# Performance work log

Hardware: AMD Instinct MI355X
Metric: run time of the kernel (lower is better)

The kernel has to match this reference:

```python
import jax, jax.numpy as jnp
import numpy as np

N, E = 100000, 3200000
IN, HID, OUT, ED = 16, 64, 32, 3
BN_EPS = 1e-5


def setup_inputs() -> dict:
    key = jax.random.key(0)
    ks = jax.random.split(key, 40)
    d = {}
    d["x"] = jax.random.normal(ks[0], (N, IN), jnp.float32)
    d["edge_index"] = jax.random.randint(ks[1], (2, E), 0, N, dtype=jnp.int32)
    d["edge_attr"] = jax.random.normal(ks[2], (E, ED), jnp.float32)
    i = [3]
    def p(shape):
        w = jax.random.normal(ks[i[0]], shape, jnp.float32) * 0.05
        i[0] += 1
        return w
    for tag, nd in (("inj1", IN), ("inj2", HID), ("inj3", HID)):
        d[tag + "_w1"] = p((ED, nd)); d[tag + "_b1"] = p((nd,))
        d[tag + "_w2"] = p((nd, nd)); d[tag + "_b2"] = p((nd,))
    for tag, ci, co in (("conv1", IN, HID), ("conv2", HID, HID), ("conv3", HID, OUT)):
        d[tag + "_wl"] = p((ci, co)); d[tag + "_bl"] = p((co,))
        d[tag + "_wr"] = p((ci, co))
    for tag, c in (("bn1", HID), ("bn2", HID), ("bn3", OUT)):
        d[tag + "_w"] = p((c,)); d[tag + "_b"] = p((c,))
    return d


def _inject(x, src, dst, edge_attr, w1, b1, w2, b2):
    # edge MLP: [E, ED] -> [E, node_dim], sigmoid wind gate from column 2
    h = jax.nn.relu(edge_attr @ w1 + b1) @ w2 + b2
    gate = jax.nn.sigmoid(edge_attr[:, 2:3])
    msg = h * gate
    agg = jax.ops.segment_sum(msg, dst, num_segments=x.shape[0])
    return x + agg


def _sage(x, src, dst, wl, bl, wr):
    # PyG SAGEConv (mean aggr): lin_l(mean_{j in N(i)} x_j) + lin_r(x_i)
    n = x.shape[0]
    s = jax.ops.segment_sum(x[src], dst, num_segments=n)
    cnt = jax.ops.segment_sum(jnp.ones((src.shape[0], 1), x.dtype), dst, num_segments=n)
    mean = s / jnp.maximum(cnt, 1.0)
    return mean @ wl + bl + x @ wr


def _bn(x, w, b):
    # eval-mode BatchNorm with running_mean=0, running_var=1
    return x * (w / jnp.sqrt(1.0 + BN_EPS)) + b


def reference(x, edge_index, edge_attr,
              inj1_w1, inj1_b1, inj1_w2, inj1_b2,
              inj2_w1, inj2_b1, inj2_w2, inj2_b2,
              inj3_w1, inj3_b1, inj3_w2, inj3_b2,
              conv1_wl, conv1_bl, conv1_wr,
              conv2_wl, conv2_bl, conv2_wr,
              conv3_wl, conv3_bl, conv3_wr,
              bn1_w, bn1_b, bn2_w, bn2_b, bn3_w, bn3_b):
    src, dst = edge_index[0], edge_index[1]
    h = _inject(x, src, dst, edge_attr, inj1_w1, inj1_b1, inj1_w2, inj1_b2)
    h = jax.nn.relu(_bn(_sage(h, src, dst, conv1_wl, conv1_bl, conv1_wr), bn1_w, bn1_b))
    h = _inject(h, src, dst, edge_attr, inj2_w1, inj2_b1, inj2_w2, inj2_b2)
    h = jax.nn.relu(_bn(_sage(h, src, dst, conv2_wl, conv2_bl, conv2_wr), bn2_w, bn2_b))
    h = _inject(h, src, dst, edge_attr, inj3_w1, inj3_b1, inj3_w2, inj3_b2)
    h = jax.nn.relu(_bn(_sage(h, src, dst, conv3_wl, conv3_bl, conv3_wr), bn3_w, bn3_b))
    return h
```

## Files before the change

kernel.cpp:

```cpp
#include <hip/hip_runtime.h>
#include <math.h>

#define N_NODES 100000
#define N_EDGES 3200000
#define NB 391
#define CHUNK 4096
#define NCHUNK 782
#define HCHUNK 4096
#define NHCHUNK 782
#define CAPB 10240

constexpr size_t al512(size_t x){ return (x + 511) & ~size_t(511); }
constexpr size_t o_bcnt = 0;
constexpr size_t o_bst  = al512(o_bcnt + 512*4);
constexpr size_t o_gb   = al512(o_bst  + 512*4);
constexpr size_t o_off  = al512(o_gb   + 512*4);
constexpr size_t o_srcp = al512(o_off  + ((size_t)N_NODES+1)*4);
constexpr size_t o_epk  = al512(o_srcp + (size_t)N_EDGES*4);
constexpr size_t o_U1   = al512(o_epk  + (size_t)N_EDGES*16);
constexpr size_t o_U2   = al512(o_U1   + (size_t)N_NODES*16*4);
constexpr size_t o_U3   = o_U2 + (size_t)N_NODES*64*4;
constexpr size_t o_gs   = al512(o_U3   + (size_t)N_NODES*64*4);
constexpr size_t o_h1   = al512(o_gs   + (size_t)N_NODES*4);
constexpr size_t o_m1   = al512(o_h1   + (size_t)N_NODES*16*4);
constexpr size_t o_rec  = o_U2;
constexpr size_t o_h2bf = o_epk;
constexpr size_t o_h3bf = o_epk + (size_t)N_NODES*128;
constexpr size_t o_m2   = o_U2;
constexpr size_t o_y3   = o_U3;
constexpr size_t o_m3p  = o_U2;

#define BN_RSQRT 0.9999950000374997f

__device__ __forceinline__ float4 ld4(const float* p){ return *(const float4*)p; }
__device__ __forceinline__ float fc(const float4& v, int i){ return ((const float*)&v)[i]; }
__device__ __forceinline__ float uf(unsigned u){ return __uint_as_float(u); }

__device__ __forceinline__ unsigned f2bf(float x){
    unsigned u = __float_as_uint(x);
    u += 0x7fffu + ((u >> 16) & 1u);
    return u >> 16;
}

__global__ __launch_bounds__(256) void khistBin(const int* __restrict__ dst,
                                                int* __restrict__ binCnt){
    __shared__ int c[NB];
    int t = threadIdx.x;
    for(int i=t; i<NB; i+=256) c[i] = 0;
    __syncthreads();
    long base = (long)blockIdx.x*HCHUNK;
    int nrem = (int)(N_EDGES - base); if(nrem > HCHUNK) nrem = HCHUNK;
    for(int k=t; k<nrem; k+=256)
        atomicAdd(&c[dst[base+k] >> 8], 1);
    __syncthreads();
    for(int i=t; i<NB; i+=256)
        if(c[i]) atomicAdd(&binCnt[i], c[i]);
}

__global__ __launch_bounds__(512) void kscanBin(const int* __restrict__ binCnt,
                                                int* __restrict__ binStart,
                                                int* __restrict__ gbase){
    __shared__ int s[512];
    int t = threadIdx.x;
    int v = (t < NB) ? binCnt[t] : 0;
    s[t] = v; __syncthreads();
    for(int off=1; off<512; off<<=1){
        int a = (t>=off) ? s[t-off] : 0;
        __syncthreads(); s[t] += a; __syncthreads();
    }
    int ex = (t==0) ? 0 : s[t-1];
    if(t < NB){ binStart[t] = ex; gbase[t] = ex; }
    if(t == NB) binStart[NB] = s[NB-1];
}

__global__ __launch_bounds__(256) void kbinA(const int* __restrict__ src,
                                             const int* __restrict__ dst,
                                             const float* __restrict__ ea,
                                             int* __restrict__ gbase,
                                             unsigned* __restrict__ recD){
    __shared__ int cnt[NB], lofs[NB], gst[NB], lcnt[NB];
    __shared__ int sscan[256];
    __shared__ unsigned stage[CHUNK*3];
    __shared__ unsigned short binOf[CHUNK];
    int t = threadIdx.x;
    long e0i = (long)blockIdx.x*CHUNK;
    int nrem = (int)(N_EDGES - e0i); if(nrem > CHUNK) nrem = CHUNK;
    if(nrem <= 0) return;

    for(int b=t; b<NB; b+=256){ cnt[b]=0; lcnt[b]=0; }
    __syncthreads();
    for(int k=t; k<nrem; k+=256)
        atomicAdd(&cnt[dst[e0i+k] >> 8], 1);
    __syncthreads();
    int c0 = (2*t   < NB) ? cnt[2*t]   : 0;
    int c1 = (2*t+1 < NB) ? cnt[2*t+1] : 0;
    sscan[t] = c0 + c1;
    __syncthreads();
    for(int off=1; off<256; off<<=1){
        int v = (t>=off) ? sscan[t-off] : 0;
        __syncthreads(); sscan[t] += v; __syncthreads();
    }
    int base = (t==0) ? 0 : sscan[t-1];
    if(2*t   < NB) lofs[2*t]   = base;
    if(2*t+1 < NB) lofs[2*t+1] = base + c0;
    for(int b=t; b<NB; b+=256){
        int c = cnt[b];
        gst[b] = c ? atomicAdd(&gbase[b], c) : 0;
    }
    __syncthreads();
    for(int k=t; k<nrem; k+=256){
        long i = e0i + k;
        int d = dst[i];
        int s = src[i];
        float a0 = ea[i*3+0], a1 = ea[i*3+1], a2 = ea[i*3+2];
        int b = d >> 8;
        int p = lofs[b] + atomicAdd(&lcnt[b], 1);
        stage[3*p+0] = (unsigned)s | ((unsigned)(d & 255) << 17);
        stage[3*p+1] = (f2bf(a1)<<16) | f2bf(a0);
        stage[3*p+2] = __float_as_uint(a2);
        binOf[p] = (unsigned short)b;
    }
    __syncthreads();
    int total3 = nrem*3;
    for(int q=t; q<total3; q+=256){
        int p = q/3;
        int r = q - 3*p;
        int b = binOf[p];
        int g = gst[b] + (p - lofs[b]);
        recD[(size_t)3*g + r] = stage[q];
    }
}

__global__ __launch_bounds__(512) void kbinB(const unsigned* __restrict__ recD,
                                             const int* __restrict__ binStart,
                                             int* __restrict__ offs,
                                             int* __restrict__ srcp,
                                             float4* __restrict__ epk){
    __shared__ int pfx[257], lcnt[256];
    __shared__ int sscan[256];
    __shared__ unsigned short perm[CAPB];
    __shared__ unsigned char  nibOf[CAPB];
    int t = threadIdx.x;
    int b = blockIdx.x;
    int n0 = b*256;
    int nn = N_NODES - n0; if(nn > 256) nn = 256;
    int base = binStart[b];
    int m    = binStart[b+1] - base;
    for(int i=t; i<256; i+=512) lcnt[i] = 0;
    __syncthreads();
    for(int p=t; p<m; p+=512){
        unsigned w0 = recD[(size_t)3*(base+p)];
        int nib = (int)((w0 >> 17) & 255u);
        if(p < CAPB) nibOf[p] = (unsigned char)nib;
        atomicAdd(&lcnt[nib], 1);
    }
    __syncthreads();
    if(t < 256) sscan[t] = lcnt[t];
    __syncthreads();
    if(t < 256){
        for(int off=1; off<256; off<<=1){
            int v = (t>=off) ? sscan[t-off] : 0;
            __syncthreads(); sscan[t] += v; __syncthreads();
        }
        pfx[t+1] = sscan[t];
        if(t==0) pfx[0] = 0;
    } else {
        for(int off=1; off<256; off<<=1){ __syncthreads(); __syncthreads(); }
    }
    __syncthreads();
    for(int i=t; i<=nn; i+=512) offs[n0+i] = base + pfx[i];
    for(int i=t; i<256; i+=512) lcnt[i] = 0;
    __syncthreads();
    for(int p=t; p<m; p+=512){
        int nib = nibOf[p];
        int slot = pfx[nib] + atomicAdd(&lcnt[nib], 1);
        perm[slot] = (unsigned short)p;
    }
    __syncthreads();
    for(int s=t; s<m; s+=512){
        size_t q = (size_t)3*(base + (int)perm[s]);
        unsigned w0 = recD[q], w1 = recD[q+1], w2 = recD[q+2];
        float e2 = uf(w2);
        float gate = __builtin_amdgcn_rcpf(1.f + __expf(-e2));
        srcp[base+s] = (int)(w0 & 0x1FFFFu);
        epk [base+s] = make_float4(uf(w1<<16), uf(w1 & 0xffff0000u), e2, gate);
    }
}

__global__ __launch_bounds__(256) void kinject(const float4* __restrict__ epk, const int* __restrict__ offs,
                        const float* __restrict__ w11, const float* __restrict__ b11,
                        const float* __restrict__ w12, const float* __restrict__ b12,
                        const float* __restrict__ w13, const float* __restrict__ b13,
                        float* __restrict__ U1, float* __restrict__ U2,
                        float* __restrict__ U3, float* __restrict__ gsum){
    int gid = blockIdx.x*blockDim.x + threadIdx.x;
    int node = gid >> 6;
    if(node >= N_NODES) return;
    int lane = threadIdx.x & 63;
    int q = lane >> 4, j = lane & 15;
    float wa1=w11[j], wb1=w11[16+j], wc1=w11[32+j], bb1=b11[j];
    float wa2[4], wb2[4], wc2[4], bv2[4], wa3[4], wb3[4], wc3[4], bv3[4];
    #pragma unroll
    for(int k=0;k<4;k++){
        int c = j + 16*k;
        wa2[k]=w12[c]; wb2[k]=w12[64+c]; wc2[k]=w12[128+c]; bv2[k]=b12[c];
        wa3[k]=w13[c]; wb3[k]=w13[64+c]; wc3[k]=w13[128+c]; bv3[k]=b13[c];
    }
    int beg = offs[node], end = offs[node+1];
    float a1=0.f, g=0.f;
    float a2[4] = {0.f,0.f,0.f,0.f};
    float a3[4] = {0.f,0.f,0.f,0.f};
    for(int e=beg; e<end; e+=8){
        int ee0 = e + q, ee1 = e + 4 + q;
        float4 r0 = make_float4(0.f,0.f,0.f,0.f);
        float4 r1 = make_float4(0.f,0.f,0.f,0.f);
        if(ee0 < end) r0 = epk[ee0];
        if(ee1 < end) r1 = epk[ee1];
        {
            float h = fmaf(r0.z,wc1, fmaf(r0.y,wb1, fmaf(r0.x,wa1, bb1)));
            a1 = fmaf(fmaxf(h,0.f), r0.w, a1);
            #pragma unroll
            for(int k=0;k<4;k++){
                float h2 = fmaf(r0.z,wc2[k], fmaf(r0.y,wb2[k], fmaf(r0.x,wa2[k], bv2[k])));
                a2[k] = fmaf(fmaxf(h2,0.f), r0.w, a2[k]);
                float h3 = fmaf(r0.z,wc3[k], fmaf(r0.y,wb3[k], fmaf(r0.x,wa3[k], bv3[k])));
                a3[k] = fmaf(fmaxf(h3,0.f), r0.w, a3[k]);
            }
            g += r0.w;
        }
        {
            float h = fmaf(r1.z,wc1, fmaf(r1.y,wb1, fmaf(r1.x,wa1, bb1)));
            a1 = fmaf(fmaxf(h,0.f), r1.w, a1);
            #pragma unroll
            for(int k=0;k<4;k++){
                float h2 = fmaf(r1.z,wc2[k], fmaf(r1.y,wb2[k], fmaf(r1.x,wa2[k], bv2[k])));
                a2[k] = fmaf(fmaxf(h2,0.f), r1.w, a2[k]);
                float h3 = fmaf(r1.z,wc3[k], fmaf(r1.y,wb3[k], fmaf(r1.x,wa3[k], bv3[k])));
                a3[k] = fmaf(fmaxf(h3,0.f), r1.w, a3[k]);
            }
            g += r1.w;
        }
    }
    #pragma unroll
    for(int k=0;k<4;k++){
        a2[k] += __shfl_xor(a2[k], 16); a2[k] += __shfl_xor(a2[k], 32);
        a3[k] += __shfl_xor(a3[k], 16); a3[k] += __shfl_xor(a3[k], 32);
    }
    a1 += __shfl_xor(a1, 16); a1 += __shfl_xor(a1, 32);
    g  += __shfl_xor(g, 16);  g  += __shfl_xor(g, 32);
    float v2 = (q==0) ? a2[0] : (q==1) ? a2[1] : (q==2) ? a2[2] : a2[3];
    float v3 = (q==0) ? a3[0] : (q==1) ? a3[1] : (q==2) ? a3[2] : a3[3];
    U2[(size_t)node*64 + lane] = v2;
    U3[(size_t)node*64 + lane] = v3;
    if(lane < 16) U1[node*16 + j] = a1;
    if(lane == 0) gsum[node] = g;
}

__global__ void kgather16(const float* __restrict__ h, const int* __restrict__ srcp,
                          const int* __restrict__ offs, float* __restrict__ m){
    int gid = blockIdx.x*blockDim.x + threadIdx.x;
    int node = gid >> 6;
    if(node >= N_NODES) return;
    int lane = threadIdx.x & 63;
    int q = lane >> 4, d = lane & 15;
    int beg = offs[node], end = offs[node+1];
    float acc = 0.f;
    for(int e=beg+q; e<end; e+=4) acc += h[(size_t)srcp[e]*16 + d];
    acc += __shfl_down(acc, 32);
    acc += __shfl_down(acc, 16);
    if(lane < 16){
        float c = fmaxf((float)(end-beg), 1.f);
        m[node*16 + lane] = acc / c;
    }
}

__global__ void kgather64bf(const unsigned* __restrict__ hbf, const int* __restrict__ srcp,
                            const int* __restrict__ offs, float* __restrict__ m){
    int gid = blockIdx.x*blockDim.x + threadIdx.x;
    int node = gid >> 6;
    if(node >= N_NODES) return;
    int lane = threadIdx.x & 63;
    int q = lane >> 4, j = lane & 15;
    int beg = offs[node], end = offs[node+1];
    float4 acc = make_float4(0.f,0.f,0.f,0.f);
    for(int e=beg; e<end; e+=4){
        int ee = e + q;
        if(ee < end){
            int s = srcp[ee];
            uint2 w = *(const uint2*)(hbf + (size_t)s*32 + 2*j);
            acc.x += uf(w.x<<16); acc.y += uf(w.x & 0xffff0000u);
            acc.z += uf(w.y<<16); acc.w += uf(w.y & 0xffff0000u);
        }
    }
    acc.x += __shfl_xor(acc.x,16); acc.x += __shfl_xor(acc.x,32);
    acc.y += __shfl_xor(acc.y,16); acc.y += __shfl_xor(acc.y,32);
    acc.z += __shfl_xor(acc.z,16); acc.z += __shfl_xor(acc.z,32);
    acc.w += __shfl_xor(acc.w,16); acc.w += __shfl_xor(acc.w,32);
    if(lane < 16){
        float inv = 1.f / fmaxf((float)(end-beg), 1.f);
        float4 o; o.x=acc.x*inv; o.y=acc.y*inv; o.z=acc.z*inv; o.w=acc.w*inv;
        *(float4*)(m + (size_t)node*64 + 4*j) = o;
    }
}

__global__ void kgather32bf(const unsigned* __restrict__ y3, const int* __restrict__ srcp,
                            const int* __restrict__ offs, float* __restrict__ m){
    int gid = blockIdx.x*blockDim.x + threadIdx.x;
    int node = gid >> 6;
    if(node >= N_NODES) return;
    int lane = threadIdx.x & 63;
    int q = lane >> 4, j = lane & 15;
    int beg = offs[node], end = offs[node+1];
    float ax=0.f, ay=0.f;
    for(int e=beg; e<end; e+=8){
        int ee0 = e + q, ee1 = e + 4 + q;
        if(ee0 < end){
            unsigned w = y3[(size_t)srcp[ee0]*16 + j];
            ax += uf(w<<16); ay += uf(w & 0xffff0000u);
        }
        if(ee1 < end){
            unsigned w = y3[(size_t)srcp[ee1]*16 + j];
            ax += uf(w<<16); ay += uf(w & 0xffff0000u);
        }
    }
    ax += __shfl_xor(ax,16); ax += __shfl_xor(ax,32);
    ay += __shfl_xor(ay,16); ay += __shfl_xor(ay,32);
    if(lane < 16){
        float inv = 1.f / fmaxf((float)(end-beg), 1.f);
        float2 o; o.x = ax*inv; o.y = ay*inv;
        *(float2*)(m + (size_t)node*32 + 2*j) = o;
    }
}


__global__ __launch_bounds__(256) void kdense0(const float* __restrict__ x, const float* __restrict__ U1,
                        const float* __restrict__ gs, const float* __restrict__ w2,
                        const float* __restrict__ b2, float* __restrict__ h1){
    __shared__ float sw[256];
    int t = threadIdx.x;
    sw[t] = w2[t];
    __syncthreads();
    int idx = blockIdx.x*256 + t;
    int n = idx >> 4, j = idx & 15;
    float acc = x[idx] + gs[n]*b2[j];
    const float4* row = (const float4*)(U1 + n*16);
    #pragma unroll
    for(int i4=0;i4<4;i4++){
        float4 r = row[i4];
        acc += r.x*sw[(i4*4+0)*16 + j];
        acc += r.y*sw[(i4*4+1)*16 + j];
        acc += r.z*sw[(i4*4+2)*16 + j];
        acc += r.w*sw[(i4*4+3)*16 + j];
    }
    h1[idx] = acc;
}

__global__ __launch_bounds__(256) void kdense1(const float* __restrict__ m1, const float* __restrict__ h1,
                        const float* __restrict__ U2, const float* __restrict__ gs,
                        const float* __restrict__ wl, const float* __restrict__ bl,
                        const float* __restrict__ wr,
                        const float* __restrict__ w2, const float* __restrict__ b2,
                        const float* __restrict__ bnw, const float* __restrict__ bnb,
                        unsigned* __restrict__ h2bf){
    __shared__ float4 swl[16*16];
    __shared__ float4 swr[16*16];
    __shared__ float4 sw2[64*16];
    int t = threadIdx.x;
    swl[t] = ((const float4*)wl)[t];
    swr[t] = ((const float4*)wr)[t];
    #pragma unroll
    for(int k=0;k<4;k++) sw2[t + 256*k] = ((const float4*)w2)[t + 256*k];
    __syncthreads();

    int w = t>>6, l = t&63;
    int jg = l&15, j0 = jg*4, ng = l>>4;
    int nb = blockIdx.x*64 + w*16 + ng*4;
    int nn[4];
    #pragma unroll
    for(int k=0;k<4;k++) nn[k] = (nb+k < N_NODES) ? nb+k : N_NODES-1;

    float a[4][4], b[4][4];
    float4 blv = ld4(bl + j0);
    float4 b2v = ld4(b2 + j0);
    #pragma unroll
    for(int k=0;k<4;k++){
        float g = gs[nn[k]];
        a[k][0]=blv.x; a[k][1]=blv.y; a[k][2]=blv.z; a[k][3]=blv.w;
        b[k][0]=g*b2v.x; b[k][1]=g*b2v.y; b[k][2]=g*b2v.z; b[k][3]=g*b2v.w;
    }
    #pragma unroll
    for(int i=0;i<16;i+=4){
        float4 rm[4], rh[4];
        #pragma unroll
        for(int k=0;k<4;k++){ rm[k] = ld4(m1 + nn[k]*16 + i); rh[k] = ld4(h1 + nn[k]*16 + i); }
        #pragma unroll
        for(int ii=0;ii<4;ii++){
            float4 wL = swl[(i+ii)*16 + jg];
            float4 wR = swr[(i+ii)*16 + jg];
            #pragma unroll
            for(int k=0;k<4;k++){
                float vm = fc(rm[k],ii), vh = fc(rh[k],ii);
                a[k][0] = fmaf(vm,wL.x, fmaf(vh,wR.x, a[k][0]));
                a[k][1] = fmaf(vm,wL.y, fmaf(vh,wR.y, a[k][1]));
                a[k][2] = fmaf(vm,wL.z, fmaf(vh,wR.z, a[k][2]));
                a[k][3] = fmaf(vm,wL.w, fmaf(vh,wR.w, a[k][3]));
            }
        }
    }
    #pragma unroll 4
    for(int i=0;i<64;i+=4){
        float4 ru[4];
        #pragma unroll
        for(int k=0;k<4;k++) ru[k] = ld4(U2 + (size_t)nn[k]*64 + i);
        #pragma unroll
        for(int ii=0;ii<4;ii++){
            float4 wv = sw2[(i+ii)*16 + jg];
            #pragma unroll
            for(int k=0;k<4;k++){
                float vu = fc(ru[k],ii);
                b[k][0] = fmaf(vu,wv.x,b[k][0]);
                b[k][1] = fmaf(vu,wv.y,b[k][1]);
                b[k][2] = fmaf(vu,wv.z,b[k][2]);
                b[k][3] = fmaf(vu,wv.w,b[k][3]);
            }
        }
    }
    float4 bw = ld4(bnw + j0), bb = ld4(bnb + j0);
    #pragma unroll
    for(int k=0;k<4;k++){
        if(nb+k < N_NODES){
            float ox = fmaxf(a[k][0]*(bw.x*BN_RSQRT)+bb.x,0.f) + b[k][0];
            float oy = fmaxf(a[k][1]*(bw.y*BN_RSQRT)+bb.y,0.f) + b[k][1];
            float oz = fmaxf(a[k][2]*(bw.z*BN_RSQRT)+bb.z,0.f) + b[k][2];
            float ow = fmaxf(a[k][3]*(bw.w*BN_RSQRT)+bb.w,0.f) + b[k][3];
            uint2 pk; pk.x = f2bf(ox) | (f2bf(oy)<<16); pk.y = f2bf(oz) | (f2bf(ow)<<16);
            *(uint2*)(h2bf + (size_t)(nb+k)*32 + (j0>>1)) = pk;
        }
    }
}

__global__ __launch_bounds__(256) void kdense2(const float* __restrict__ m2, const unsigned* __restrict__ h2bf,
                        const float* __restrict__ U3, const float* __restrict__ gs,
                        const float* __restrict__ wl, const float* __restrict__ bl,
                        const float* __restrict__ wr,
                        const float* __restrict__ w2, const float* __restrict__ b2,
                        const float* __restrict__ bnw, const float* __restrict__ bnb,
                        unsigned* __restrict__ h3bf){
    __shared__ float4 swl[64*16];
    __shared__ float4 swr[64*16];
    __shared__ float4 sw2[64*16];
    int t = threadIdx.x;
    #pragma unroll
    for(int k=0;k<4;k++){
        swl[t + 256*k] = ((const float4*)wl)[t + 256*k];
        swr[t + 256*k] = ((const float4*)wr)[t + 256*k];
        sw2[t + 256*k] = ((const float4*)w2)[t + 256*k];
    }
    __syncthreads();

    int w = t>>6, l = t&63;
    int jg = l&15, j0 = jg*4, ng = l>>4;
    int nb = blockIdx.x*64 + w*16 + ng*4;
    int nn[4];
    #pragma unroll
    for(int k=0;k<4;k++) nn[k] = (nb+k < N_NODES) ? nb+k : N_NODES-1;

    float a[4][4], b[4][4];
    float4 blv = ld4(bl + j0);
    float4 b2v = ld4(b2 + j0);
    #pragma unroll
    for(int k=0;k<4;k++){
        float g = gs[nn[k]];
        a[k][0]=blv.x; a[k][1]=blv.y; a[k][2]=blv.z; a[k][3]=blv.w;
        b[k][0]=g*b2v.x; b[k][1]=g*b2v.y; b[k][2]=g*b2v.z; b[k][3]=g*b2v.w;
    }
    #pragma unroll 4
    for(int i=0;i<64;i+=4){
        float4 rm[4], rh[4];
        #pragma unroll
        for(int k=0;k<4;k++){
            rm[k] = ld4(m2 + (size_t)nn[k]*64 + i);
            uint2 hw = *(const uint2*)(h2bf + (size_t)nn[k]*32 + (i>>1));
            rh[k].x = uf(hw.x<<16); rh[k].y = uf(hw.x & 0xffff0000u);
            rh[k].z = uf(hw.y<<16); rh[k].w = uf(hw.y & 0xffff0000u);
        }
        #pragma unroll
        for(int ii=0;ii<4;ii++){
            float4 wL = swl[(i+ii)*16 + jg];
            float4 wR = swr[(i+ii)*16 + jg];
            #pragma unroll
            for(int k=0;k<4;k++){
                float vm = fc(rm[k],ii), vh = fc(rh[k],ii);
                a[k][0] = fmaf(vm,wL.x, fmaf(vh,wR.x, a[k][0]));
                a[k][1] = fmaf(vm,wL.y, fmaf(vh,wR.y, a[k][1]));
                a[k][2] = fmaf(vm,wL.z, fmaf(vh,wR.z, a[k][2]));
                a[k][3] = fmaf(vm,wL.w, fmaf(vh,wR.w, a[k][3]));
            }
        }
    }
    #pragma unroll 4
    for(int i=0;i<64;i+=4){
        float4 ru[4];
        #pragma unroll
        for(int k=0;k<4;k++) ru[k] = ld4(U3 + (size_t)nn[k]*64 + i);
        #pragma unroll
        for(int ii=0;ii<4;ii++){
            float4 wv = sw2[(i+ii)*16 + jg];
            #pragma unroll
            for(int k=0;k<4;k++){
                float vu = fc(ru[k],ii);
                b[k][0] = fmaf(vu,wv.x,b[k][0]);
                b[k][1] = fmaf(vu,wv.y,b[k][1]);
                b[k][2] = fmaf(vu,wv.z,b[k][2]);
                b[k][3] = fmaf(vu,wv.w,b[k][3]);
            }
        }
    }
    float4 bw = ld4(bnw + j0), bb = ld4(bnb + j0);
    #pragma unroll
    for(int k=0;k<4;k++){
        if(nb+k < N_NODES){
            float ox = fmaxf(a[k][0]*(bw.x*BN_RSQRT)+bb.x,0.f) + b[k][0];
            float oy = fmaxf(a[k][1]*(bw.y*BN_RSQRT)+bb.y,0.f) + b[k][1];
            float oz = fmaxf(a[k][2]*(bw.z*BN_RSQRT)+bb.z,0.f) + b[k][2];
            float ow = fmaxf(a[k][3]*(bw.w*BN_RSQRT)+bb.w,0.f) + b[k][3];
            uint2 pk; pk.x = f2bf(ox) | (f2bf(oy)<<16); pk.y = f2bf(oz) | (f2bf(ow)<<16);
            *(uint2*)(h3bf + (size_t)(nb+k)*32 + (j0>>1)) = pk;
        }
    }
}

__global__ __launch_bounds__(256) void kproj3(const unsigned* __restrict__ h3bf,
                                              const float* __restrict__ wl,
                                              unsigned* __restrict__ y3){
    __shared__ float4 swl[64*8];
    int t = threadIdx.x;
    #pragma unroll
    for(int k=0;k<2;k++) swl[t + 256*k] = ((const float4*)wl)[t + 256*k];
    __syncthreads();

    int w = t>>6, l = t&63;
    int jg = l&7, j0 = jg*4, ng = l>>3;
    int nb = blockIdx.x*128 + w*32 + ng*4;
    int nn[4];
    #pragma unroll
    for(int k=0;k<4;k++) nn[k] = (nb+k < N_NODES) ? nb+k : N_NODES-1;

    float a[4][4];
    #pragma unroll
    for(int k=0;k<4;k++){ a[k][0]=0.f; a[k][1]=0.f; a[k][2]=0.f; a[k][3]=0.f; }
    #pragma unroll 4
    for(int i=0;i<64;i+=4){
        float4 rh[4];
        #pragma unroll
        for(int k=0;k<4;k++){
            uint2 hw = *(const uint2*)(h3bf + (size_t)nn[k]*32 + (i>>1));
            rh[k].x = uf(hw.x<<16); rh[k].y = uf(hw.x & 0xffff0000u);
            rh[k].z = uf(hw.y<<16); rh[k].w = uf(hw.y & 0xffff0000u);
        }
        #pragma unroll
        for(int ii=0;ii<4;ii++){
            float4 wL = swl[(i+ii)*8 + jg];
            #pragma unroll
            for(int k=0;k<4;k++){
                float vh = fc(rh[k],ii);
                a[k][0] = fmaf(vh,wL.x,a[k][0]);
                a[k][1] = fmaf(vh,wL.y,a[k][1]);
                a[k][2] = fmaf(vh,wL.z,a[k][2]);
                a[k][3] = fmaf(vh,wL.w,a[k][3]);
            }
        }
    }
    #pragma unroll
    for(int k=0;k<4;k++){
        if(nb+k < N_NODES){
            uint2 pk;
            pk.x = f2bf(a[k][0]) | (f2bf(a[k][1])<<16);
            pk.y = f2bf(a[k][2]) | (f2bf(a[k][3])<<16);
            *(uint2*)(y3 + (size_t)(nb+k)*16 + (j0>>1)) = pk;
        }
    }
}

__global__ __launch_bounds__(256) void kdense3(const float* __restrict__ m3p, const unsigned* __restrict__ h3bf,
                        const float* __restrict__ bl,
                        const float* __restrict__ wr,
                        const float* __restrict__ bnw, const float* __restrict__ bnb,
                        float* __restrict__ out){
    __shared__ float4 swr[64*8];
    int t = threadIdx.x;
    #pragma unroll
    for(int k=0;k<2;k++) swr[t + 256*k] = ((const float4*)wr)[t + 256*k];
    __syncthreads();

    int w = t>>6, l = t&63;
    int jg = l&7, j0 = jg*4, ng = l>>3;
    int nb = blockIdx.x*128 + w*32 + ng*4;
    int nn[4];
    #pragma unroll
    for(int k=0;k<4;k++) nn[k] = (nb+k < N_NODES) ? nb+k : N_NODES-1;

    float a[4][4];
    float4 blv = ld4(bl + j0);
    #pragma unroll
    for(int k=0;k<4;k++){
        float4 mp = ld4(m3p + (size_t)nn[k]*32 + j0);
        a[k][0]=blv.x+mp.x; a[k][1]=blv.y+mp.y; a[k][2]=blv.z+mp.z; a[k][3]=blv.w+mp.w;
    }
    #pragma unroll 4
    for(int i=0;i<64;i+=4){
        float4 rh[4];
        #pragma unroll
        for(int k=0;k<4;k++){
            uint2 hw = *(const uint2*)(h3bf + (size_t)nn[k]*32 + (i>>1));
            rh[k].x = uf(hw.x<<16); rh[k].y = uf(hw.x & 0xffff0000u);
            rh[k].z = uf(hw.y<<16); rh[k].w = uf(hw.y & 0xffff0000u);
        }
        #pragma unroll
        for(int ii=0;ii<4;ii++){
            float4 wR = swr[(i+ii)*8 + jg];
            #pragma unroll
            for(int k=0;k<4;k++){
                float vh = fc(rh[k],ii);
                a[k][0] = fmaf(vh,wR.x,a[k][0]);
                a[k][1] = fmaf(vh,wR.y,a[k][1]);
                a[k][2] = fmaf(vh,wR.z,a[k][2]);
                a[k][3] = fmaf(vh,wR.w,a[k][3]);
            }
        }
    }
    float4 bw = ld4(bnw + j0), bb = ld4(bnb + j0);
    #pragma unroll
    for(int k=0;k<4;k++){
        if(nb+k < N_NODES){
            float4 o;
            o.x = fmaxf(a[k][0]*(bw.x*BN_RSQRT)+bb.x,0.f);
            o.y = fmaxf(a[k][1]*(bw.y*BN_RSQRT)+bb.y,0.f);
            o.z = fmaxf(a[k][2]*(bw.z*BN_RSQRT)+bb.z,0.f);
            o.w = fmaxf(a[k][3]*(bw.w*BN_RSQRT)+bb.w,0.f);
            *(float4*)(out + (size_t)(nb+k)*32 + j0) = o;
        }
    }
}

extern "C" void kernel_launch(void* const* d_in, const int* in_sizes, int n_in,
                              void* d_out, int out_size, void* d_ws, size_t ws_size,
                              hipStream_t stream){
    const float* x    = (const float*)d_in[0];
    const int*   ei   = (const int*)  d_in[1];
    const float* ea   = (const float*)d_in[2];
    const float* i1w1 = (const float*)d_in[3];
    const float* i1b1 = (const float*)d_in[4];
    const float* i1w2 = (const float*)d_in[5];
    const float* i1b2 = (const float*)d_in[6];
    const float* i2w1 = (const float*)d_in[7];
    const float* i2b1 = (const float*)d_in[8];
    const float* i2w2 = (const float*)d_in[9];
    const float* i2b2 = (const float*)d_in[10];
    const float* i3w1 = (const float*)d_in[11];
    const float* i3b1 = (const float*)d_in[12];
    const float* i3w2 = (const float*)d_in[13];
    const float* i3b2 = (const float*)d_in[14];
    const float* c1wl = (const float*)d_in[15];
    const float* c1bl = (const float*)d_in[16];
    const float* c1wr = (const float*)d_in[17];
    const float* c2wl = (const float*)d_in[18];
    const float* c2bl = (const float*)d_in[19];
    const float* c2wr = (const float*)d_in[20];
    const float* c3wl = (const float*)d_in[21];
    const float* c3bl = (const float*)d_in[22];
    const float* c3wr = (const float*)d_in[23];
    const float* bn1w = (const float*)d_in[24];
    const float* bn1b = (const float*)d_in[25];
    const float* bn2w = (const float*)d_in[26];
    const float* bn2b = (const float*)d_in[27];
    const float* bn3w = (const float*)d_in[28];
    const float* bn3b = (const float*)d_in[29];

    char* ws = (char*)d_ws;
    int*      bcnt = (int*)     (ws + o_bcnt);
    int*      bst  = (int*)     (ws + o_bst);
    int*      gb   = (int*)     (ws + o_gb);
    int*      offs = (int*)     (ws + o_off);
    int*      srcp = (int*)     (ws + o_srcp);
    float4*   epk  = (float4*)  (ws + o_epk);
    unsigned* recD = (unsigned*)(ws + o_rec);
    float*    U1   = (float*)   (ws + o_U1);
    float*    U2   = (float*)   (ws + o_U2);
    float*    U3   = (float*)   (ws + o_U3);
    float*    gs   = (float*)   (ws + o_gs);
    float*    h1   = (float*)   (ws + o_h1);
    float*    m1   = (float*)   (ws + o_m1);
    unsigned* h2bf = (unsigned*)(ws + o_h2bf);
    unsigned* h3bf = (unsigned*)(ws + o_h3bf);
    float*    m2   = (float*)   (ws + o_m2);
    unsigned* y3   = (unsigned*)(ws + o_y3);
    float*    m3p  = (float*)   (ws + o_m3p);

    const int* src = ei;
    const int* dst = ei + N_EDGES;

    hipMemsetAsync(bcnt, 0, 512*4, stream);
    khistBin <<<NHCHUNK, 256, 0, stream>>>(dst, bcnt);
    kscanBin <<<1,       512, 0, stream>>>(bcnt, bst, gb);
    kbinA  <<<NCHUNK, 256, 0, stream>>>(src, dst, ea, gb, recD);
    kbinB  <<<NB,     512, 0, stream>>>(recD, bst, offs, srcp, epk);

    kinject <<<N_NODES/4, 256, 0, stream>>>(epk, offs,
                                            i1w1, i1b1, i2w1, i2b1, i3w1, i3b1,
                                            U1, U2, U3, gs);
    kdense0 <<<N_NODES*16/256, 256, 0, stream>>>(x, U1, gs, i1w2, i1b2, h1);
    kgather16<<<N_NODES/4, 256, 0, stream>>>(h1, srcp, offs, m1);
    kdense1 <<<(N_NODES+63)/64, 256, 0, stream>>>(m1, h1, U2, gs,
                                                 c1wl, c1bl, c1wr, i2w2, i2b2,
                                                 bn1w, bn1b, h2bf);
    kgather64bf<<<N_NODES/4, 256, 0, stream>>>(h2bf, srcp, offs, m2);
    kdense2 <<<(N_NODES+63)/64, 256, 0, stream>>>(m2, h2bf, U3, gs,
                                                 c2wl, c2bl, c2wr, i3w2, i3b2,
                                                 bn2w, bn2b, h3bf);
    kproj3  <<<(N_NODES+127)/128, 256, 0, stream>>>(h3bf, c3wl, y3);
    kgather32bf<<<N_NODES/4, 256, 0, stream>>>(y3, srcp, offs, m3p);
    kdense3 <<<(N_NODES+127)/128, 256, 0, stream>>>(m3p, h3bf, c3bl, c3wr,
                                                 bn3w, bn3b, (float*)d_out);
}
```

Baseline: 750.3 us.

## Fuse conv3 projection into dense2 and peel full-edge loops in gathers

Folds the kproj3 projection into kdense2. The freshly computed h3 tile goes to shared memory and is multiplied by conv3's lin_l weights in the same block, which removes a kernel launch and a re-read of h3 from global memory. y3 is moved to the U1 buffer, presumably to avoid aliasing U3 while kdense2 still reads it. The edge loops in kinject, kgather64bf and kgather32bf are split into an unpredicated main loop over full groups of 8 edges plus a guarded tail, and kinject gets an occupancy hint in launch_bounds. The cost is more shared memory and an extra sync in kdense2, which may lower its occupancy.

```diff
diff --git a/kernel.cpp b/kernel.cpp
--- a/kernel.cpp
+++ b/kernel.cpp
@@ -27,7 +27,7 @@
 constexpr size_t o_h2bf = o_epk;
 constexpr size_t o_h3bf = o_epk + (size_t)N_NODES*128;
 constexpr size_t o_m2   = o_U2;
-constexpr size_t o_y3   = o_U3;
+constexpr size_t o_y3   = o_U1;
 constexpr size_t o_m3p  = o_U2;
 
 #define BN_RSQRT 0.9999950000374997f
@@ -187,7 +187,19 @@
     }
 }
 
-__global__ __launch_bounds__(256) void kinject(const float4* __restrict__ epk, const int* __restrict__ offs,
+#define EDGE_ACC(r) { \
+    float h_ = fmaf((r).z,wc1, fmaf((r).y,wb1, fmaf((r).x,wa1, bb1))); \
+    a1 = fmaf(fmaxf(h_,0.f), (r).w, a1); \
+    _Pragma("unroll") \
+    for(int k_=0;k_<4;k_++){ \
+        float h2_ = fmaf((r).z,wc2[k_], fmaf((r).y,wb2[k_], fmaf((r).x,wa2[k_], bv2[k_]))); \
+        a2[k_] = fmaf(fmaxf(h2_,0.f), (r).w, a2[k_]); \
+        float h3_ = fmaf((r).z,wc3[k_], fmaf((r).y,wb3[k_], fmaf((r).x,wa3[k_], bv3[k_]))); \
+        a3[k_] = fmaf(fmaxf(h3_,0.f), (r).w, a3[k_]); \
+    } \
+    g += (r).w; }
+
+__global__ __launch_bounds__(256,4) void kinject(const float4* __restrict__ epk, const int* __restrict__ offs,
                         const float* __restrict__ w11, const float* __restrict__ b11,
                         const float* __restrict__ w12, const float* __restrict__ b12,
                         const float* __restrict__ w13, const float* __restrict__ b13,
@@ -210,36 +222,20 @@
     float a1=0.f, g=0.f;
     float a2[4] = {0.f,0.f,0.f,0.f};
     float a3[4] = {0.f,0.f,0.f,0.f};
-    for(int e=beg; e<end; e+=8){
+    int e = beg;
+    int efull = beg + ((end - beg) & ~7);
+    for(; e < efull; e+=8){
+        float4 r0 = epk[e + q];
+        float4 r1 = epk[e + 4 + q];
+        EDGE_ACC(r0);
+        EDGE_ACC(r1);
+    }
+    if(e < end){
         int ee0 = e + q, ee1 = e + 4 + q;
-        float4 r0 = make_float4(0.f,0.f,0.f,0.f);
-        float4 r1 = make_float4(0.f,0.f,0.f,0.f);
-        if(ee0 < end) r0 = epk[ee0];
-        if(ee1 < end) r1 = epk[ee1];
-        {
-            float h = fmaf(r0.z,wc1, fmaf(r0.y,wb1, fmaf(r0.x,wa1, bb1)));
-            a1 = fmaf(fmaxf(h,0.f), r0.w, a1);
-            #pragma unroll
-            for(int k=0;k<4;k++){
-                float h2 = fmaf(r0.z,wc2[k], fmaf(r0.y,wb2[k], fmaf(r0.x,wa2[k], bv2[k])));
-                a2[k] = fmaf(fmaxf(h2,0.f), r0.w, a2[k]);
-                float h3 = fmaf(r0.z,wc3[k], fmaf(r0.y,wb3[k], fmaf(r0.x,wa3[k], bv3[k])));
-                a3[k] = fmaf(fmaxf(h3,0.f), r0.w, a3[k]);
-            }
-            g += r0.w;
-        }
-        {
-            float h = fmaf(r1.z,wc1, fmaf(r1.y,wb1, fmaf(r1.x,wa1, bb1)));
-            a1 = fmaf(fmaxf(h,0.f), r1.w, a1);
-            #pragma unroll
-            for(int k=0;k<4;k++){
-                float h2 = fmaf(r1.z,wc2[k], fmaf(r1.y,wb2[k], fmaf(r1.x,wa2[k], bv2[k])));
-                a2[k] = fmaf(fmaxf(h2,0.f), r1.w, a2[k]);
-                float h3 = fmaf(r1.z,wc3[k], fmaf(r1.y,wb3[k], fmaf(r1.x,wa3[k], bv3[k])));
-                a3[k] = fmaf(fmaxf(h3,0.f), r1.w, a3[k]);
-            }
-            g += r1.w;
-        }
+        float4 r0 = (ee0 < end) ? epk[ee0] : make_float4(0.f,0.f,0.f,0.f);
+        float4 r1 = (ee1 < end) ? epk[ee1] : make_float4(0.f,0.f,0.f,0.f);
+        EDGE_ACC(r0);
+        EDGE_ACC(r1);
     }
     #pragma unroll
     for(int k=0;k<4;k++){
@@ -283,7 +279,18 @@
     int q = lane >> 4, j = lane & 15;
     int beg = offs[node], end = offs[node+1];
     float4 acc = make_float4(0.f,0.f,0.f,0.f);
-    for(int e=beg; e<end; e+=4){
+    int e = beg;
+    int efull = beg + ((end - beg) & ~7);
+    for(; e < efull; e+=8){
+        int s0 = srcp[e + q], s1 = srcp[e + 4 + q];
+        uint2 w0 = *(const uint2*)(hbf + (size_t)s0*32 + 2*j);
+        uint2 w1 = *(const uint2*)(hbf + (size_t)s1*32 + 2*j);
+        acc.x += uf(w0.x<<16); acc.y += uf(w0.x & 0xffff0000u);
+        acc.z += uf(w0.y<<16); acc.w += uf(w0.y & 0xffff0000u);
+        acc.x += uf(w1.x<<16); acc.y += uf(w1.x & 0xffff0000u);
+        acc.z += uf(w1.y<<16); acc.w += uf(w1.y & 0xffff0000u);
+    }
+    for(; e < end; e+=4){
         int ee = e + q;
         if(ee < end){
             int s = srcp[ee];
@@ -312,14 +319,18 @@
     int q = lane >> 4, j = lane & 15;
     int beg = offs[node], end = offs[node+1];
     float ax=0.f, ay=0.f;
-    for(int e=beg; e<end; e+=8){
-        int ee0 = e + q, ee1 = e + 4 + q;
-        if(ee0 < end){
-            unsigned w = y3[(size_t)srcp[ee0]*16 + j];
-            ax += uf(w<<16); ay += uf(w & 0xffff0000u);
-        }
-        if(ee1 < end){
-            unsigned w = y3[(size_t)srcp[ee1]*16 + j];
+    int e = beg;
+    int efull = beg + ((end - beg) & ~7);
+    for(; e < efull; e+=8){
+        unsigned w0 = y3[(size_t)srcp[e + q]*16 + j];
+        unsigned w1 = y3[(size_t)srcp[e + 4 + q]*16 + j];
+        ax += uf(w0<<16); ay += uf(w0 & 0xffff0000u);
+        ax += uf(w1<<16); ay += uf(w1 & 0xffff0000u);
+    }
+    for(; e < end; e+=4){
+        int ee = e + q;
+        if(ee < end){
+            unsigned w = y3[(size_t)srcp[ee]*16 + j];
             ax += uf(w<<16); ay += uf(w & 0xffff0000u);
         }
     }
@@ -445,10 +456,13 @@
                         const float* __restrict__ wr,
                         const float* __restrict__ w2, const float* __restrict__ b2,
                         const float* __restrict__ bnw, const float* __restrict__ bnb,
-                        unsigned* __restrict__ h3bf){
+                        const float* __restrict__ wl3,
+                        unsigned* __restrict__ h3bf, unsigned* __restrict__ y3){
     __shared__ float4 swl[64*16];
     __shared__ float4 swr[64*16];
     __shared__ float4 sw2[64*16];
+    __shared__ float4 swl3[64*8];
+    __shared__ unsigned sh3[64*32];
     int t = threadIdx.x;
     #pragma unroll
     for(int k=0;k<4;k++){
@@ -456,11 +470,14 @@
         swr[t + 256*k] = ((const float4*)wr)[t + 256*k];
         sw2[t + 256*k] = ((const float4*)w2)[t + 256*k];
     }
+    swl3[t] = ((const float4*)wl3)[t];
+    swl3[t+256] = ((const float4*)wl3)[t+256];
     __syncthreads();
 
     int w = t>>6, l = t&63;
     int jg = l&15, j0 = jg*4, ng = l>>4;
-    int nb = blockIdx.x*64 + w*16 + ng*4;
+    int ln0 = w*16 + ng*4;
+    int nb = blockIdx.x*64 + ln0;
     int nn[4];
     #pragma unroll
     for(int k=0;k<4;k++) nn[k] = (nb+k < N_NODES) ? nb+k : N_NODES-1;
@@ -519,66 +536,43 @@
     float4 bw = ld4(bnw + j0), bb = ld4(bnb + j0);
     #pragma unroll
     for(int k=0;k<4;k++){
-        if(nb+k < N_NODES){
-            float ox = fmaxf(a[k][0]*(bw.x*BN_RSQRT)+bb.x,0.f) + b[k][0];
-            float oy = fmaxf(a[k][1]*(bw.y*BN_RSQRT)+bb.y,0.f) + b[k][1];
-            float oz = fmaxf(a[k][2]*(bw.z*BN_RSQRT)+bb.z,0.f) + b[k][2];
-            float ow = fmaxf(a[k][3]*(bw.w*BN_RSQRT)+bb.w,0.f) + b[k][3];
-            uint2 pk; pk.x = f2bf(ox) | (f2bf(oy)<<16); pk.y = f2bf(oz) | (f2bf(ow)<<16);
+        float ox = fmaxf(a[k][0]*(bw.x*BN_RSQRT)+bb.x,0.f) + b[k][0];
+        float oy = fmaxf(a[k][1]*(bw.y*BN_RSQRT)+bb.y,0.f) + b[k][1];
+        float oz = fmaxf(a[k][2]*(bw.z*BN_RSQRT)+bb.z,0.f) + b[k][2];
+        float ow = fmaxf(a[k][3]*(bw.w*BN_RSQRT)+bb.w,0.f) + b[k][3];
+        uint2 pk; pk.x = f2bf(ox) | (f2bf(oy)<<16); pk.y = f2bf(oz) | (f2bf(ow)<<16);
+        *(uint2*)(sh3 + (ln0+k)*32 + (j0>>1)) = pk;
+        if(nb+k < N_NODES)
             *(uint2*)(h3bf + (size_t)(nb+k)*32 + (j0>>1)) = pk;
-        }
-    }
-}
-
-__global__ __launch_bounds__(256) void kproj3(const unsigned* __restrict__ h3bf,
-                                              const float* __restrict__ wl,
-                                              unsigned* __restrict__ y3){
-    __shared__ float4 swl[64*8];
-    int t = threadIdx.x;
-    #pragma unroll
-    for(int k=0;k<2;k++) swl[t + 256*k] = ((const float4*)wl)[t + 256*k];
-    __syncthreads();
-
-    int w = t>>6, l = t&63;
-    int jg = l&7, j0 = jg*4, ng = l>>3;
-    int nb = blockIdx.x*128 + w*32 + ng*4;
-    int nn[4];
-    #pragma unroll
-    for(int k=0;k<4;k++) nn[k] = (nb+k < N_NODES) ? nb+k : N_NODES-1;
-
-    float a[4][4];
-    #pragma unroll
-    for(int k=0;k<4;k++){ a[k][0]=0.f; a[k][1]=0.f; a[k][2]=0.f; a[k][3]=0.f; }
-    #pragma unroll 4
-    for(int i=0;i<64;i+=4){
-        float4 rh[4];
-        #pragma unroll
-        for(int k=0;k<4;k++){
-            uint2 hw = *(const uint2*)(h3bf + (size_t)nn[k]*32 + (i>>1));
-            rh[k].x = uf(hw.x<<16); rh[k].y = uf(hw.x & 0xffff0000u);
-            rh[k].z = uf(hw.y<<16); rh[k].w = uf(hw.y & 0xffff0000u);
-        }
-        #pragma unroll
-        for(int ii=0;ii<4;ii++){
-            float4 wL = swl[(i+ii)*8 + jg];
-            #pragma unroll
-            for(int k=0;k<4;k++){
-                float vh = fc(rh[k],ii);
-                a[k][0] = fmaf(vh,wL.x,a[k][0]);
-                a[k][1] = fmaf(vh,wL.y,a[k][1]);
-                a[k][2] = fmaf(vh,wL.z,a[k][2]);
-                a[k][3] = fmaf(vh,wL.w,a[k][3]);
-            }
-        }
-    }
-    #pragma unroll
-    for(int k=0;k<4;k++){
-        if(nb+k < N_NODES){
-            uint2 pk;
-            pk.x = f2bf(a[k][0]) | (f2bf(a[k][1])<<16);
-            pk.y = f2bf(a[k][2]) | (f2bf(a[k][3])<<16);
-            *(uint2*)(y3 + (size_t)(nb+k)*16 + (j0>>1)) = pk;
-        }
+    }
+    __syncthreads();
+    int nl = t >> 2, jc = t & 3;
+    int gnode = blockIdx.x*64 + nl;
+    if(gnode < N_NODES){
+        float y[8] = {0.f,0.f,0.f,0.f,0.f,0.f,0.f,0.f};
+        #pragma unroll 8
+        for(int i2=0; i2<32; ++i2){
+            unsigned hw = sh3[nl*32 + i2];
+            float h0 = uf(hw<<16), h1 = uf(hw & 0xffff0000u);
+            float4 A0 = swl3[(2*i2)*8 + jc*2];
+            float4 A1 = swl3[(2*i2)*8 + jc*2 + 1];
+            float4 B0 = swl3[(2*i2+1)*8 + jc*2];
+            float4 B1 = swl3[(2*i2+1)*8 + jc*2 + 1];
+            y[0] = fmaf(h0,A0.x, fmaf(h1,B0.x, y[0]));
+            y[1] = fmaf(h0,A0.y, fmaf(h1,B0.y, y[1]));
+            y[2] = fmaf(h0,A0.z, fmaf(h1,B0.z, y[2]));
+            y[3] = fmaf(h0,A0.w, fmaf(h1,B0.w, y[3]));
+            y[4] = fmaf(h0,A1.x, fmaf(h1,B1.x, y[4]));
+            y[5] = fmaf(h0,A1.y, fmaf(h1,B1.y, y[5]));
+            y[6] = fmaf(h0,A1.z, fmaf(h1,B1.z, y[6]));
+            y[7] = fmaf(h0,A1.w, fmaf(h1,B1.w, y[7]));
+        }
+        uint4 pk;
+        pk.x = f2bf(y[0]) | (f2bf(y[1])<<16);
+        pk.y = f2bf(y[2]) | (f2bf(y[3])<<16);
+        pk.z = f2bf(y[4]) | (f2bf(y[5])<<16);
+        pk.w = f2bf(y[6]) | (f2bf(y[7])<<16);
+        *(uint4*)(y3 + (size_t)gnode*16 + jc*4) = pk;
     }
 }
 
@@ -717,8 +711,7 @@
     kgather64bf<<<N_NODES/4, 256, 0, stream>>>(h2bf, srcp, offs, m2);
     kdense2 <<<(N_NODES+63)/64, 256, 0, stream>>>(m2, h2bf, U3, gs,
                                                  c2wl, c2bl, c2wr, i3w2, i3b2,
-                                                 bn2w, bn2b, h3bf);
-    kproj3  <<<(N_NODES+127)/128, 256, 0, stream>>>(h3bf, c3wl, y3);
+                                                 bn2w, bn2b, c3wl, h3bf, y3);
     kgather32bf<<<N_NODES/4, 256, 0, stream>>>(y3, srcp, offs, m3p);
     kdense3 <<<(N_NODES+127)/128, 256, 0, stream>>>(m3p, h3bf, c3bl, c3wr,
                                                  bn3w, bn3b, (float*)d_out);
```

New measurement: 685.6 us. -8.6%, faster.
